# Kernel optimization log

Measured on AMD Instinct MI355X. Metric: run time of the kernel, lower is better.

Reference implementation:

```python
import jax, jax.numpy as jnp
import numpy as np

D = 256      # d_model
H = 4        # n_heads
DK = 64      # d_k
DV = 64      # d_v
L = 2        # n_layers
B = 128      # batch of episodes
LN_EPS = 1e-5


def _layer_norm(x, g, b):
    mu = jnp.mean(x, axis=-1, keepdims=True)
    var = jnp.mean(jnp.square(x - mu), axis=-1, keepdims=True)
    return (x - mu) / jnp.sqrt(var + LN_EPS) * g + b


def _category_matrix(N, K):
    """[S,S] int matrix of weight categories, vectorizing the Python loop in
    get_attn_weight. Categories index into the (6,) attn_weight vector:
    0=same_sample, 1=same_class, 2=diff_class, 3=s_to_query, 4=query_to_s, 5=query."""
    NK = N * K
    S = NK + 1
    r = jnp.arange(S)[:, None]
    c = jnp.arange(S)[None, :]
    sup_r = r < NK
    sup_c = c < NK
    cat = jnp.full((S, S), 2, dtype=jnp.int32)                      # w_diff_class
    cat = jnp.where(sup_r & (c == NK), 3, cat)                       # w_stoquery (last col)
    cat = jnp.where(sup_r & sup_c & ((r // K) == (c // K)), 1, cat)  # w_same_class block
    cat = jnp.where(sup_r & (r == c), 0, cat)                        # w_same_sample diag
    cat = jnp.where((r == NK) & (c < NK), 4, cat)                    # w_querytos (last row)
    cat = jnp.where((r == NK) & (c == NK), 5, cat)                   # w_query
    return cat


def setup_inputs() -> dict:
    key = jax.random.key(0)
    ks = jax.random.split(key, 32)
    N, K = 20, 25
    S = N * K + 1
    std_k = np.sqrt(2.0 / (D + DK)).astype(np.float32)
    std_v = np.sqrt(2.0 / (D + DV)).astype(np.float32)
    xav = lambda k, sh: jax.random.normal(k, sh, jnp.float32) * np.sqrt(2.0 / (sh[-2] + sh[-1])).astype(np.float32)
    d = {
        "samples": jax.random.normal(ks[0], (B, S, D), jnp.float32),
        "Wq": jax.random.normal(ks[1], (L, D, H * DK), jnp.float32) * std_k,
        "Wk": jax.random.normal(ks[2], (L, D, H * DK), jnp.float32) * std_k,
        "Wv": jax.random.normal(ks[3], (L, D, H * DV), jnp.float32) * std_v,
        "attn_w": jax.random.uniform(ks[4], (L, H, 6), jnp.float32, -0.7, 0.7),  # xavier-tanh-ish
        "mha_fc_w": xav(ks[5], (L, D, D)),
        "mha_fc_b": jnp.zeros((L, D), jnp.float32),
        "mha_ln_g": jnp.ones((L, D), jnp.float32),
        "mha_ln_b": jnp.zeros((L, D), jnp.float32),
        "d_fc1_w": xav(ks[6], (L, D, D)),
        "d_fc1_b": jnp.zeros((L, D), jnp.float32),
        "d_fc2_w": xav(ks[7], (L, D, D)),
        "d_fc2_b": jnp.zeros((L, D), jnp.float32),
        "d_ln_g": jnp.ones((L, D), jnp.float32),
        "d_ln_b": jnp.zeros((L, D), jnp.float32),
        "out_fc_w": xav(ks[8], (D, D)),
        "out_fc_b": jnp.zeros((D,), jnp.float32),
        "out_ln_g": jnp.ones((D,), jnp.float32),
        "out_ln_b": jnp.zeros((D,), jnp.float32),
        "N": N,
        "K": K,
    }
    return d


def reference(samples, Wq, Wk, Wv, attn_w, mha_fc_w, mha_fc_b, mha_ln_g, mha_ln_b,
              d_fc1_w, d_fc1_b, d_fc2_w, d_fc2_b, d_ln_g, d_ln_b,
              out_fc_w, out_fc_b, out_ln_g, out_ln_b, N, K):
    temperature = np.sqrt(DK).astype(np.float32)
    cat = _category_matrix(N, K)  # [S,S] int32
    original = samples
    x = samples
    for l in range(L):
        residual = x
        Bsz, S, _ = x.shape
        q = (x @ Wq[l]).reshape(Bsz, S, H, DK)
        k = (x @ Wk[l]).reshape(Bsz, S, H, DK)
        v = (x @ Wv[l]).reshape(Bsz, S, H, DV)
        # per-head scaled-dot attention, all heads vectorized: [B,H,S,S]
        attn = jnp.einsum('bqhd,bkhd->bhqk', q, k) / temperature
        attn = jax.nn.softmax(attn, axis=-1)
        # block-structured learnt gate: tanh(weight_matrix) per head
        gate = jnp.tanh(attn_w[l][:, cat])          # [H,S,S]
        attn = gate[None] * attn                    # [B,H,S,S]
        out = jnp.einsum('bhqk,bkhd->bqhd', attn, v).reshape(Bsz, S, H * DV)
        out = out @ mha_fc_w[l] + mha_fc_b[l]
        x = _layer_norm(out + residual, mha_ln_g[l], mha_ln_b[l])
        # Dense FFN with residual
        h = jax.nn.relu(x @ d_fc1_w[l] + d_fc1_b[l])
        h = h @ d_fc2_w[l] + d_fc2_b[l]
        x = _layer_norm(h + x, d_ln_g[l], d_ln_b[l])
    # nlayers > 1 final projection + residual to original input
    x = x @ out_fc_w + out_fc_b
    x = _layer_norm(x + original, out_ln_g, out_ln_b)
    return x
```

## Files before the change

kernel.cpp:

```cpp
#include <hip/hip_runtime.h>
#include <cstdint>
#include <cstddef>
#include <cmath>

#define D 256
#define H 4
#define LN_EPS 1e-5f
#define SPAD 512
#define NMAT 13
#define PBS 520
#define LOG2E 1.44269504088896340736f

typedef __attribute__((ext_vector_type(8))) short short8;
typedef __attribute__((ext_vector_type(4))) short short4v;
typedef __attribute__((ext_vector_type(4))) float f32x4;
typedef __attribute__((ext_vector_type(2))) float f32x2;
typedef __attribute__((ext_vector_type(4))) int i32x4;

static __device__ __forceinline__ short f2bf(float f) {
    union { float f; unsigned u; } a; a.f = f;
    unsigned r = a.u + 0x7fffu + ((a.u >> 16) & 1u);
    return (short)(r >> 16);
}

static __device__ __forceinline__ float exp2_fast(float x) {
#if __has_builtin(__builtin_amdgcn_exp2f)
    return __builtin_amdgcn_exp2f(x);
#else
    float r; asm("v_exp_f32 %0, %1" : "=v"(r) : "v"(x)); return r;
#endif
}

static __device__ __forceinline__ int idivf(int x, int Kc, float rKc) {
    int q = (int)((float)x * rKc);
    q -= (q * Kc > x) ? 1 : 0;
    q += ((q + 1) * Kc <= x) ? 1 : 0;
    return q;
}

struct PackArgs { const float* src[NMAT]; float scale[NMAT]; short* dst; };

__global__ __launch_bounds__(256)
void pack_kernel(PackArgs pa)
{
    const int mat = blockIdx.y;
    const int el = blockIdx.x * 256 + threadIdx.x;
    const int n = el & 255, k = el >> 8;
    const int nt = n >> 4, l16 = n & 15;
    const int kc = k >> 5, qd = (k >> 3) & 3, j = k & 7;
    const size_t didx = (((size_t)(kc * 16 + nt) * 64) + qd * 16 + l16) * 8 + j;
    pa.dst[(size_t)mat * 65536 + didx] =
        f2bf(pa.src[mat][(size_t)k * 256 + n] * pa.scale[mat]);
}

__global__ __launch_bounds__(256)
void gate_cls_kernel(const float* __restrict__ aw, const int* __restrict__ Kp,
                     float* __restrict__ gc, int S)
{
    const int idx = blockIdx.x * 256 + threadIdx.x;
    const int h = blockIdx.y, l = blockIdx.z;
    const int cls = idx >> 9, pos = idx & 511;
    const int key = (pos & ~31) | ((pos & 1) << 4) | ((pos >> 1) & 15);
    const int NK = S - 1;
    const int Kc = Kp[0];
    int cat;
    if (cls < 20) cat = (key == NK) ? 3 : ((key < NK && key / Kc == cls) ? 1 : 2);
    else          cat = (key == NK) ? 5 : 4;
    gc[((size_t)(l * H + h) * 21 + cls) * 512 + pos] = tanhf(aw[(l * H + h) * 6 + cat]);
}

__global__ __launch_bounds__(256)
void cast_kernel(const float* __restrict__ x, short* __restrict__ xb, long n)
{
    const long i = ((long)blockIdx.x * 256 + threadIdx.x) * 4;
    if (i >= n) return;
    const f32x4 v = *(const f32x4*)(x + i);
    short4v o;
    o.x = f2bf(v.x); o.y = f2bf(v.y); o.z = f2bf(v.z); o.w = f2bf(v.w);
    *(short4v*)(xb + i) = o;
}

static __device__ __forceinline__ void gemm_tile_lds(const short* __restrict__ A,
                                                     const short* __restrict__ Bt,
                                                     short (&Bs)[2][8192],
                                                     int rowA, int tid, int lane, int quad,
                                                     f32x4 (&acc)[16])
{
    const short* Ar = A + (size_t)rowA * D + quad * 8;
    #pragma unroll
    for (int nt = 0; nt < 16; ++nt) acc[nt] = (f32x4){0.f, 0.f, 0.f, 0.f};
    {
        const short8* src = (const short8*)Bt + tid;
        short8* dst = (short8*)Bs[0] + tid;
        dst[0] = src[0]; dst[512] = src[512];
    }
    __syncthreads();
    #pragma unroll
    for (int kc = 0; kc < 8; ++kc) {
        short8 stg0, stg1;
        if (kc < 7) {
            const short8* src = (const short8*)(Bt + (size_t)(kc + 1) * 8192) + tid;
            stg0 = src[0]; stg1 = src[512];
        }
        const short8 af = *(const short8*)(Ar + kc * 32);
        const short* Bl = Bs[kc & 1] + lane * 8;
        #pragma unroll
        for (int nt = 0; nt < 16; ++nt) {
            const short8 bf = *(const short8*)(Bl + nt * 512);
            acc[nt] = __builtin_amdgcn_mfma_f32_16x16x32_bf16(af, bf, acc[nt], 0, 0, 0);
        }
        if (kc < 7) {
            short8* dst = (short8*)Bs[(kc + 1) & 1] + tid;
            dst[0] = stg0; dst[512] = stg1;
        }
        __syncthreads();
    }
}

__global__ __launch_bounds__(512)
void gemm_res_ln_kernel(const short* __restrict__ A, const short* __restrict__ Bt,
                        const float* __restrict__ bias, const float* __restrict__ resid,
                        const float* __restrict__ gam, const float* __restrict__ bet,
                        float* __restrict__ xout, short* __restrict__ xbout)
{
    const int tid = threadIdx.x, wave = tid >> 6, lane = tid & 63;
    const int l16 = lane & 15, quad = lane >> 4;
    const int row0 = blockIdx.x * 128 + wave * 16;
    __shared__ __align__(16) short Bs[2][8192];
    f32x4 acc[16];
    gemm_tile_lds(A, Bt, Bs, row0 + l16, tid, lane, quad, acc);

    #pragma unroll
    for (int nt = 0; nt < 16; ++nt) {
        const int col = nt * 16 + l16;
        const float bl = bias[col];
        #pragma unroll
        for (int r = 0; r < 4; ++r)
            acc[nt][r] += bl + resid[(size_t)(row0 + quad * 4 + r) * D + col];
    }
    float mu[4], rstd[4];
    #pragma unroll
    for (int r = 0; r < 4; ++r) {
        float s = 0.f;
        #pragma unroll
        for (int nt = 0; nt < 16; ++nt) s += acc[nt][r];
        s += __shfl_xor(s, 1, 64); s += __shfl_xor(s, 2, 64);
        s += __shfl_xor(s, 4, 64); s += __shfl_xor(s, 8, 64);
        mu[r] = s * (1.f / D);
        float q = 0.f;
        #pragma unroll
        for (int nt = 0; nt < 16; ++nt) { const float d = acc[nt][r] - mu[r]; q = fmaf(d, d, q); }
        q += __shfl_xor(q, 1, 64); q += __shfl_xor(q, 2, 64);
        q += __shfl_xor(q, 4, 64); q += __shfl_xor(q, 8, 64);
        rstd[r] = rsqrtf(q * (1.f / D) + LN_EPS);
    }
    #pragma unroll
    for (int nt = 0; nt < 16; ++nt) {
        const int col = nt * 16 + l16;
        const float g = gam[col], be = bet[col];
        #pragma unroll
        for (int r = 0; r < 4; ++r) {
            const size_t idx = (size_t)(row0 + quad * 4 + r) * D + col;
            const float o = (acc[nt][r] - mu[r]) * rstd[r] * g + be;
            xout[idx] = o;
            xbout[idx] = f2bf(o);
        }
    }
}

__global__ __launch_bounds__(512)
void gemm_relu_kernel(const short* __restrict__ A, const short* __restrict__ Bt,
                      const float* __restrict__ bias, short* __restrict__ hb)
{
    const int tid = threadIdx.x, wave = tid >> 6, lane = tid & 63;
    const int l16 = lane & 15, quad = lane >> 4;
    const int row0 = blockIdx.x * 128 + wave * 16;
    __shared__ __align__(16) short Bs[2][8192];
    f32x4 acc[16];
    gemm_tile_lds(A, Bt, Bs, row0 + l16, tid, lane, quad, acc);
    #pragma unroll
    for (int nt = 0; nt < 16; ++nt) {
        const int col = nt * 16 + l16;
        const float bl = bias[col];
        #pragma unroll
        for (int r = 0; r < 4; ++r)
            hb[(size_t)(row0 + quad * 4 + r) * D + col] = f2bf(fmaxf(acc[nt][r] + bl, 0.f));
    }
}

__global__ __launch_bounds__(512)
void qkv_gemm_kernel(const short* __restrict__ A, const short* __restrict__ Wt,
                     short* __restrict__ Qb, short* __restrict__ Kb,
                     short* __restrict__ Vb, int S)
{
    const int tid = threadIdx.x, wave = tid >> 6, lane = tid & 63;
    const int l16 = lane & 15, quad = lane >> 4;
    const int row0 = blockIdx.x * 128 + wave * 16;
    __shared__ __align__(16) short Bs[2][8192];
    int bb[4], ss[4];
    #pragma unroll
    for (int r = 0; r < 4; ++r) {
        const int row = row0 + quad * 4 + r;
        bb[r] = row / S; ss[r] = row - bb[r] * S;
    }
    #pragma unroll 1
    for (int m = 0; m < 3; ++m) {
        f32x4 acc[16];
        gemm_tile_lds(A, Wt + (size_t)m * 65536, Bs, row0 + l16, tid, lane, quad, acc);
        #pragma unroll
        for (int nt = 0; nt < 16; ++nt) {
            const int col = nt * 16 + l16, h = col >> 6, dim = col & 63;
            #pragma unroll
            for (int r = 0; r < 4; ++r) {
                const int bh = bb[r] * H + h;
                const short v = f2bf(acc[nt][r]);
                if (m == 0)      Qb[((size_t)bh * SPAD + ss[r]) * 64 + dim] = v;
                else if (m == 1) Kb[((size_t)bh * SPAD + ss[r]) * 64 + dim] = v;
                else             Vb[((size_t)bh * S + ss[r]) * 64 + dim] = v;
            }
        }
    }
}

__global__ __launch_bounds__(256)
void vt_transpose_kernel(const short* __restrict__ Vb, short* __restrict__ Vt, int S)
{
    const int bh = blockIdx.y;
    const int s0 = blockIdx.x * 64;
    const int t = threadIdx.x;
    __shared__ short T[64][72];
    {
        const int r = t >> 2, c = (t & 3) * 16;
        const int s = s0 + r;
        short8 v0 = (short8){0,0,0,0,0,0,0,0}, v1 = (short8){0,0,0,0,0,0,0,0};
        if (s < S) {
            const short* src = Vb + ((size_t)bh * S + s) * 64 + c;
            v0 = *(const short8*)src;
            v1 = *(const short8*)(src + 8);
        }
        *(short8*)&T[r][c] = v0;
        *(short8*)&T[r][c + 8] = v1;
    }
    __syncthreads();
    {
        const int dim = t >> 2, g = t & 3;
        int w[8];
        #pragma unroll
        for (int j = 0; j < 8; ++j) {
            const int d = g * 8 + j;
            const int k0 = ((d >> 4) << 5) | (d & 15);
            const unsigned lo = (unsigned short)T[k0][dim];
            const unsigned hi = (unsigned short)T[k0 + 16][dim];
            w[j] = (int)(lo | (hi << 16));
        }
        int* dst = (int*)(Vt + ((size_t)bh * 64 + dim) * SPAD + s0) + g * 8;
        *(i32x4*)dst = (i32x4){w[0], w[1], w[2], w[3]};
        *(i32x4*)(dst + 4) = (i32x4){w[4], w[5], w[6], w[7]};
    }
}

__global__ __launch_bounds__(256, 2)
void attn_kernel(const short* __restrict__ Qb, const short* __restrict__ Kb,
                 const short* __restrict__ Vt, const float* __restrict__ gc,
                 const float* __restrict__ awl, const int* __restrict__ Kp,
                 short* __restrict__ out, int S)
{
    const int bh = blockIdx.x;
    const int qh = blockIdx.y;
    const int b = bh >> 2, h = bh & 3;
    const int tid = threadIdx.x;
    const int wave = tid >> 6, lane = tid & 63;
    const int l16 = lane & 15, quad = lane >> 4;
    const int NK = S - 1;
    const int Kc = Kp[0];
    const float rKc = 1.0f / (float)Kc;
    const float g0 = tanhf(awl[h * 6]);

    __shared__ __align__(16) float Lw[2][16][4];
    __shared__ __align__(16) short Pb[2][16][PBS];

    const int kb0 = wave * 128;
    const short* Kbh = Kb + (size_t)bh * SPAD * 64;
    const short* Vbh = Vt + (size_t)bh * 64 * SPAD;
    const float* gch = gc + (size_t)h * (21 * 512);
    const int dsl = wave * 16;
    const short* Vrow = Vbh + (size_t)(dsl + l16) * SPAD + quad * 8;

    short8 kf[16];
    #pragma unroll
    for (int c = 0; c < 4; ++c) {
        const size_t kr = (size_t)(kb0 + c * 32 + l16) * 64 + quad * 8;
        kf[4 * c + 0] = *(const short8*)(Kbh + kr);
        kf[4 * c + 1] = *(const short8*)(Kbh + kr + 32);
        kf[4 * c + 2] = *(const short8*)(Kbh + kr + 16 * 64);
        kf[4 * c + 3] = *(const short8*)(Kbh + kr + 16 * 64 + 32);
    }
    short8 vf[16];
    #pragma unroll
    for (int ks = 0; ks < 16; ++ks) vf[ks] = *(const short8*)(Vrow + ks * 32);

    #pragma unroll 1
    for (int it = 0; it < 16; ++it) {
        const int q0 = (qh * 16 + it) << 4;
        const int bsel = it & 1;

        const size_t qrow = ((size_t)bh * SPAD + q0 + l16) * 64;
        const short8 aq0 = *(const short8*)(Qb + qrow + quad * 8);
        const short8 aq1 = *(const short8*)(Qb + qrow + 32 + quad * 8);

        f32x4 sc[8];
        #pragma unroll
        for (int c = 0; c < 4; ++c) {
            const int kbase = kb0 + c * 32;
            f32x4 s0 = (f32x4){0.f, 0.f, 0.f, 0.f}, s1 = (f32x4){0.f, 0.f, 0.f, 0.f};
            s0 = __builtin_amdgcn_mfma_f32_16x16x32_bf16(aq0, kf[4 * c + 0], s0, 0, 0, 0);
            s0 = __builtin_amdgcn_mfma_f32_16x16x32_bf16(aq1, kf[4 * c + 1], s0, 0, 0, 0);
            s1 = __builtin_amdgcn_mfma_f32_16x16x32_bf16(aq0, kf[4 * c + 2], s1, 0, 0, 0);
            s1 = __builtin_amdgcn_mfma_f32_16x16x32_bf16(aq1, kf[4 * c + 3], s1, 0, 0, 0);
            if (kbase + 32 > S) {
                const bool v0 = (kbase + l16) < S, v1 = (kbase + 16 + l16) < S;
                #pragma unroll
                for (int r = 0; r < 4; ++r) {
                    s0[r] = v0 ? s0[r] : -INFINITY;
                    s1[r] = v1 ? s1[r] : -INFINITY;
                }
            }
            sc[2 * c] = s0; sc[2 * c + 1] = s1;
        }

        int dq[4]; const float* gr[4];
        #pragma unroll
        for (int r = 0; r < 4; ++r) {
            const int q = q0 + quad * 4 + r;
            const bool qs = q < NK;
            const int cls = qs ? idivf(q, Kc, rKc) : 20;
            gr[r] = gch + (size_t)cls * 512 + kb0 + 2 * l16;
            dq[r] = qs ? q : -1;
        }
        f32x2 gpre[16];
        #pragma unroll
        for (int r = 0; r < 4; ++r)
            #pragma unroll
            for (int c = 0; c < 4; ++c)
                gpre[r * 4 + c] = *(const f32x2*)(gr[r] + c * 32);

        float ls[4] = {0.f, 0.f, 0.f, 0.f};
        #pragma unroll
        for (int j = 0; j < 8; ++j) {
            #pragma unroll
            for (int r = 0; r < 4; ++r) {
                const float e = exp2_fast(sc[j][r]);
                sc[j][r] = e;
                ls[r] += e;
            }
        }
        #pragma unroll
        for (int r = 0; r < 4; ++r) {
            ls[r] += __shfl_xor(ls[r], 1, 64);
            ls[r] += __shfl_xor(ls[r], 2, 64);
            ls[r] += __shfl_xor(ls[r], 4, 64);
            ls[r] += __shfl_xor(ls[r], 8, 64);
        }
        if (l16 == 0) {
            #pragma unroll
            for (int r = 0; r < 4; ++r) Lw[bsel][quad * 4 + r][wave] = ls[r];
        }

        #pragma unroll
        for (int c = 0; c < 4; ++c) {
            const int key0 = kb0 + c * 32 + l16, key1 = key0 + 16;
            #pragma unroll
            for (int r = 0; r < 4; ++r) {
                const f32x2 g = gpre[r * 4 + c];
                const float gx = (key0 == dq[r]) ? g0 : g.x;
                const float gy = (key1 == dq[r]) ? g0 : g.y;
                const float p0 = sc[2 * c][r] * gx;
                const float p1 = sc[2 * c + 1][r] * gy;
                unsigned int pk;
                asm("v_cvt_pk_bf16_f32 %0, %1, %2" : "=v"(pk) : "v"(p0), "v"(p1));
                *(unsigned int*)(&Pb[bsel][quad * 4 + r][kb0 + c * 32 + 2 * l16]) = pk;
            }
        }
        __syncthreads();

        const short* Prow = &Pb[bsel][l16][quad * 8];
        short8 ap[16];
        #pragma unroll
        for (int ks = 0; ks < 16; ++ks) ap[ks] = *(const short8*)(Prow + ks * 32);
        f32x4 O0 = (f32x4){0.f, 0.f, 0.f, 0.f}, O1 = (f32x4){0.f, 0.f, 0.f, 0.f};
        #pragma unroll
        for (int ks = 0; ks < 16; ks += 2) {
            O0 = __builtin_amdgcn_mfma_f32_16x16x32_bf16(ap[ks], vf[ks], O0, 0, 0, 0);
            O1 = __builtin_amdgcn_mfma_f32_16x16x32_bf16(ap[ks + 1], vf[ks + 1], O1, 0, 0, 0);
        }
        const f32x4 O = O0 + O1;

        #pragma unroll
        for (int r = 0; r < 4; ++r) {
            const int q = quad * 4 + r;
            const int s = q0 + q;
            if (s < S) {
                const f32x4 lv = *(const f32x4*)Lw[bsel][q];
                const float lq = (lv[0] + lv[1]) + (lv[2] + lv[3]);
                out[((size_t)b * S + s) * D + h * 64 + dsl + l16] =
                    f2bf(O[r] * __builtin_amdgcn_rcpf(lq));
            }
        }
    }
}

extern "C" void kernel_launch(void* const* d_in, const int* in_sizes, int n_in,
                              void* d_out, int out_size, void* d_ws, size_t ws_size,
                              hipStream_t stream)
{
    const float* samples = (const float*)d_in[0];
    const float* Wq      = (const float*)d_in[1];
    const float* Wk      = (const float*)d_in[2];
    const float* Wv      = (const float*)d_in[3];
    const float* attn_w  = (const float*)d_in[4];
    const float* fc_w    = (const float*)d_in[5];
    const float* fc_b    = (const float*)d_in[6];
    const float* mha_g   = (const float*)d_in[7];
    const float* mha_b   = (const float*)d_in[8];
    const float* w1      = (const float*)d_in[9];
    const float* b1      = (const float*)d_in[10];
    const float* w2      = (const float*)d_in[11];
    const float* b2      = (const float*)d_in[12];
    const float* dg      = (const float*)d_in[13];
    const float* db      = (const float*)d_in[14];
    const float* ow      = (const float*)d_in[15];
    const float* ob      = (const float*)d_in[16];
    const float* og      = (const float*)d_in[17];
    const float* obeta   = (const float*)d_in[18];
    const int*   Kp      = (const int*)d_in[20];

    const int Bsz = 128;
    const int S = in_sizes[0] / (Bsz * D);
    const int rows = Bsz * S;
    const size_t n_el = (size_t)rows * D;
    const size_t n_pad = (size_t)Bsz * H * SPAD * 64;

    float* x   = (float*)d_out;
    short* xb  = (short*)d_ws;
    short* aob = xb + n_el;
    short* hb  = aob;
    short* Vb  = aob;
    short* Qb  = aob + n_el;
    short* Kb  = Qb + n_pad;
    short* Vt  = Kb + n_pad;
    short* wts = Vt + n_pad;
    float* gcls = (float*)(wts + (size_t)NMAT * 65536);

    PackArgs pa;
    for (int l = 0; l < 2; ++l) {
        const size_t wo = (size_t)l * 65536;
        pa.src[l*6 + 0] = Wq + wo;   pa.scale[l*6 + 0] = 0.125f * LOG2E;
        pa.src[l*6 + 1] = Wk + wo;   pa.scale[l*6 + 1] = 1.f;
        pa.src[l*6 + 2] = Wv + wo;   pa.scale[l*6 + 2] = 1.f;
        pa.src[l*6 + 3] = fc_w + wo; pa.scale[l*6 + 3] = 1.f;
        pa.src[l*6 + 4] = w1 + wo;   pa.scale[l*6 + 4] = 1.f;
        pa.src[l*6 + 5] = w2 + wo;   pa.scale[l*6 + 5] = 1.f;
    }
    pa.src[12] = ow; pa.scale[12] = 1.f;
    pa.dst = wts;
    pack_kernel<<<dim3(256, NMAT), 256, 0, stream>>>(pa);

    gate_cls_kernel<<<dim3(42, H, 2), 256, 0, stream>>>(attn_w, Kp, gcls, S);

    cast_kernel<<<(int)((n_el / 4 + 255) / 256), 256, 0, stream>>>(samples, xb, (long)n_el);

    const int gblocks = rows / 128;
    for (int l = 0; l < 2; ++l) {
        short* wl = wts + (size_t)l * 6 * 65536;
        const float* layer_in = (l == 0) ? samples : x;
        qkv_gemm_kernel<<<gblocks, 512, 0, stream>>>(xb, wl, Qb, Kb, Vb, S);
        vt_transpose_kernel<<<dim3(8, Bsz * H), 256, 0, stream>>>(Vb, Vt, S);
        attn_kernel<<<dim3(Bsz * H, 2), 256, 0, stream>>>(Qb, Kb, Vt,
                                              gcls + (size_t)l * H * 21 * 512,
                                              attn_w + (size_t)l * H * 6, Kp, aob, S);
        gemm_res_ln_kernel<<<gblocks, 512, 0, stream>>>(aob, wl + 3 * 65536,
                                              fc_b + (size_t)l * D, layer_in,
                                              mha_g + (size_t)l * D, mha_b + (size_t)l * D,
                                              x, xb);
        gemm_relu_kernel<<<gblocks, 512, 0, stream>>>(xb, wl + 4 * 65536,
                                              b1 + (size_t)l * D, hb);
        gemm_res_ln_kernel<<<gblocks, 512, 0, stream>>>(hb, wl + 5 * 65536,
                                              b2 + (size_t)l * D, x,
                                              dg + (size_t)l * D, db + (size_t)l * D,
                                              x, xb);
    }
    gemm_res_ln_kernel<<<gblocks, 512, 0, stream>>>(xb, wts + 12 * 65536,
                                              ob, samples, og, obeta, x, xb);
}
```

Before: 769.3 us.

## Preload A fragments in GEMMs; prefetch Q and merge attention query halves

The GEMM helpers now load the whole 16x256 A-row fragment into registers before the K loop, so the QKV kernel loads it once and reuses it across its three weight matrices. The attention kernel stops splitting query tiles across two blocks per (batch, head): each block walks all 32 tiles and prefetches the next tile's Q fragments while computing the current one. This removes redundant K/V fragment loads and hides Q load latency, but halves the attention grid (512 blocks) and adds register pressure.

```diff
diff --git a/kernel.cpp b/kernel.cpp
--- a/kernel.cpp
+++ b/kernel.cpp
@@ -80,13 +80,12 @@
     *(short4v*)(xb + i) = o;
 }
 
-static __device__ __forceinline__ void gemm_tile_lds(const short* __restrict__ A,
+static __device__ __forceinline__ void gemm_tile_lds(const short8 (&af)[8],
                                                      const short* __restrict__ Bt,
                                                      short (&Bs)[2][8192],
-                                                     int rowA, int tid, int lane, int quad,
+                                                     int tid, int lane,
                                                      f32x4 (&acc)[16])
 {
-    const short* Ar = A + (size_t)rowA * D + quad * 8;
     #pragma unroll
     for (int nt = 0; nt < 16; ++nt) acc[nt] = (f32x4){0.f, 0.f, 0.f, 0.f};
     {
@@ -102,12 +101,11 @@
             const short8* src = (const short8*)(Bt + (size_t)(kc + 1) * 8192) + tid;
             stg0 = src[0]; stg1 = src[512];
         }
-        const short8 af = *(const short8*)(Ar + kc * 32);
         const short* Bl = Bs[kc & 1] + lane * 8;
         #pragma unroll
         for (int nt = 0; nt < 16; ++nt) {
             const short8 bf = *(const short8*)(Bl + nt * 512);
-            acc[nt] = __builtin_amdgcn_mfma_f32_16x16x32_bf16(af, bf, acc[nt], 0, 0, 0);
+            acc[nt] = __builtin_amdgcn_mfma_f32_16x16x32_bf16(af[kc], bf, acc[nt], 0, 0, 0);
         }
         if (kc < 7) {
             short8* dst = (short8*)Bs[(kc + 1) & 1] + tid;
@@ -115,6 +113,14 @@
         }
         __syncthreads();
     }
+}
+
+static __device__ __forceinline__ void load_afrag(const short* __restrict__ A,
+                                                  int rowA, int quad, short8 (&af)[8])
+{
+    const short* Ar = A + (size_t)rowA * D + quad * 8;
+    #pragma unroll
+    for (int kc = 0; kc < 8; ++kc) af[kc] = *(const short8*)(Ar + kc * 32);
 }
 
 __global__ __launch_bounds__(512)
@@ -127,8 +133,10 @@
     const int l16 = lane & 15, quad = lane >> 4;
     const int row0 = blockIdx.x * 128 + wave * 16;
     __shared__ __align__(16) short Bs[2][8192];
+    short8 af[8];
+    load_afrag(A, row0 + l16, quad, af);
     f32x4 acc[16];
-    gemm_tile_lds(A, Bt, Bs, row0 + l16, tid, lane, quad, acc);
+    gemm_tile_lds(af, Bt, Bs, tid, lane, acc);
 
     #pragma unroll
     for (int nt = 0; nt < 16; ++nt) {
@@ -176,8 +184,10 @@
     const int l16 = lane & 15, quad = lane >> 4;
     const int row0 = blockIdx.x * 128 + wave * 16;
     __shared__ __align__(16) short Bs[2][8192];
+    short8 af[8];
+    load_afrag(A, row0 + l16, quad, af);
     f32x4 acc[16];
-    gemm_tile_lds(A, Bt, Bs, row0 + l16, tid, lane, quad, acc);
+    gemm_tile_lds(af, Bt, Bs, tid, lane, acc);
     #pragma unroll
     for (int nt = 0; nt < 16; ++nt) {
         const int col = nt * 16 + l16;
@@ -203,10 +213,12 @@
         const int row = row0 + quad * 4 + r;
         bb[r] = row / S; ss[r] = row - bb[r] * S;
     }
+    short8 af[8];
+    load_afrag(A, row0 + l16, quad, af);
     #pragma unroll 1
     for (int m = 0; m < 3; ++m) {
         f32x4 acc[16];
-        gemm_tile_lds(A, Wt + (size_t)m * 65536, Bs, row0 + l16, tid, lane, quad, acc);
+        gemm_tile_lds(af, Wt + (size_t)m * 65536, Bs, tid, lane, acc);
         #pragma unroll
         for (int nt = 0; nt < 16; ++nt) {
             const int col = nt * 16 + l16, h = col >> 6, dim = col & 63;
@@ -266,7 +278,6 @@
                  short* __restrict__ out, int S)
 {
     const int bh = blockIdx.x;
-    const int qh = blockIdx.y;
     const int b = bh >> 2, h = bh & 3;
     const int tid = threadIdx.x;
     const int wave = tid >> 6, lane = tid & 63;
@@ -299,14 +310,14 @@
     #pragma unroll
     for (int ks = 0; ks < 16; ++ks) vf[ks] = *(const short8*)(Vrow + ks * 32);
 
+    const size_t qbase = (size_t)bh * SPAD * 64;
+    short8 aq0 = *(const short8*)(Qb + qbase + (size_t)l16 * 64 + quad * 8);
+    short8 aq1 = *(const short8*)(Qb + qbase + (size_t)l16 * 64 + 32 + quad * 8);
+
     #pragma unroll 1
-    for (int it = 0; it < 16; ++it) {
-        const int q0 = (qh * 16 + it) << 4;
+    for (int it = 0; it < 32; ++it) {
+        const int q0 = it << 4;
         const int bsel = it & 1;
-
-        const size_t qrow = ((size_t)bh * SPAD + q0 + l16) * 64;
-        const short8 aq0 = *(const short8*)(Qb + qrow + quad * 8);
-        const short8 aq1 = *(const short8*)(Qb + qrow + 32 + quad * 8);
 
         f32x4 sc[8];
         #pragma unroll
@@ -328,6 +339,10 @@
             sc[2 * c] = s0; sc[2 * c + 1] = s1;
         }
 
+        const size_t nqrow = qbase + (size_t)(q0 + 16 + l16) * 64;
+        const short8 nq0 = *(const short8*)(Qb + nqrow + quad * 8);
+        const short8 nq1 = *(const short8*)(Qb + nqrow + 32 + quad * 8);
+
         int dq[4]; const float* gr[4];
         #pragma unroll
         for (int r = 0; r < 4; ++r) {
@@ -406,6 +421,8 @@
                     f2bf(O[r] * __builtin_amdgcn_rcpf(lq));
             }
         }
+
+        aq0 = nq0; aq1 = nq1;
     }
 }
 
@@ -475,7 +492,7 @@
         const float* layer_in = (l == 0) ? samples : x;
         qkv_gemm_kernel<<<gblocks, 512, 0, stream>>>(xb, wl, Qb, Kb, Vb, S);
         vt_transpose_kernel<<<dim3(8, Bsz * H), 256, 0, stream>>>(Vb, Vt, S);
-        attn_kernel<<<dim3(Bsz * H, 2), 256, 0, stream>>>(Qb, Kb, Vt,
+        attn_kernel<<<Bsz * H, 256, 0, stream>>>(Qb, Kb, Vt,
                                               gcls + (size_t)l * H * 21 * 512,
                                               attn_w + (size_t)l * H * 6, Kp, aob, S);
         gemm_res_ln_kernel<<<gblocks, 512, 0, stream>>>(aob, wl + 3 * 65536,
```

New measurement: 760.7 us. No clear change (-1.1%).
